# Optimization experiments

Measured on AMD Instinct MI355X. Metric: run time of the kernel, lower is better.

The kernel has to match this reference:

```python
import jax, jax.numpy as jnp
import numpy as np


def setup_inputs() -> dict:
    key = jax.random.key(0)
    ks = jax.random.split(key, 8)
    N, T, U = 8, 512, 64
    E, D, J, V = 512, 512, 512, 500
    s = 0.02
    return {
        "encoder_out": jax.random.normal(ks[0], (N, T, E), jnp.float32),
        "decoder_out": jax.random.normal(ks[1], (N, U, D), jnp.float32),
        "W_enc": jax.random.normal(ks[2], (J, E), jnp.float32) * s,
        "b_enc": jnp.zeros((J,), jnp.float32),
        "W_dec": jax.random.normal(ks[3], (J, D), jnp.float32) * s,
        "b_dec": jnp.zeros((J,), jnp.float32),
        "W_out": jax.random.normal(ks[4], (V, J), jnp.float32) * s,
        "b_out": jnp.zeros((V,), jnp.float32),
    }


def reference(encoder_out, decoder_out, W_enc, b_enc, W_dec, b_dec, W_out, b_out):
    # Project encoder [N,T,E]->[N,T,J] and decoder [N,U,D]->[N,U,J]
    enc = jnp.einsum("nte,je->ntj", encoder_out, W_enc) + b_enc
    dec = jnp.einsum("nud,jd->nuj", decoder_out, W_dec) + b_dec
    # Broadcast add over (T,U), tanh, then vocab projection -> [N,T,U,V]
    activations = jnp.tanh(enc[:, :, None, :] + dec[:, None, :, :])
    logits = jnp.einsum("ntuj,vj->ntuv", activations, W_out) + b_out
    return logits
```

## Files before the change

kernel.cpp:

```cpp
#include <hip/hip_runtime.h>
#include <hip/hip_bf16.h>


typedef __attribute__((ext_vector_type(4))) float f32x4;
typedef __attribute__((ext_vector_type(16))) float f32x16;
typedef __attribute__((ext_vector_type(4))) short s16x4;
typedef __attribute__((ext_vector_type(8))) short s16x8;
typedef __attribute__((ext_vector_type(8))) unsigned short u16x8;

static __device__ __forceinline__ unsigned short f2bf(float x) {
    union { float f; unsigned u; } v; v.f = x;
    return (unsigned short)((v.u + 0x7FFFu + ((v.u >> 16) & 1u)) >> 16);
}

static __device__ __forceinline__ float bf2f(unsigned short u) {
    union { unsigned u; float f; } v; v.u = ((unsigned)u) << 16;
    return v.f;
}

static __device__ __forceinline__ float fast_tanh(float x) {
    float e = __expf(2.0f * x);
    float r = __builtin_amdgcn_rcpf(e + 1.0f);
    return __builtin_fmaf(-2.0f, r, 1.0f);
}

static __device__ __forceinline__ void lbar() {
    asm volatile("s_waitcnt lgkmcnt(0)" ::: "memory");
    __builtin_amdgcn_s_barrier();
    __builtin_amdgcn_sched_barrier(0);
}

static __device__ __forceinline__ unsigned swz64(int r, int c) {
    return (unsigned)(r * 64 + ((c ^ ((r >> 1) & 3)) << 4));
}

static __device__ void proj_body(
    const float* __restrict__ A, const float* __restrict__ W,
    const float* __restrict__ b, unsigned short* __restrict__ C,
    int mt, int jt, unsigned short* As, unsigned short* Bs)
{
    const int tid = threadIdx.x;
    const int lane = tid & 63, wid = tid >> 6;
    const int wm = wid >> 1, wn = wid & 1;

    f32x4 acc[4][4];
    const f32x4 zero = {0.f, 0.f, 0.f, 0.f};
    #pragma unroll
    for (int i = 0; i < 4; ++i)
        #pragma unroll
        for (int j = 0; j < 4; ++j) acc[i][j] = zero;

    const int c8 = (tid & 7) * 8;
    const int rbase = tid >> 3;

    for (int kt = 0; kt < 8; ++kt) {
        __syncthreads();
        #pragma unroll
        for (int p = 0; p < 4; ++p) {
            int r = p * 32 + rbase;
            int byte = (r * 128 + c8 * 2) ^ ((r & 7) << 4);
            {
                const float* s = A + (size_t)(mt * 128 + r) * 512 + kt * 64 + c8;
                f32x4 v0 = *(const f32x4*)s, v1 = *(const f32x4*)(s + 4);
                s16x8 pk;
                pk[0] = (short)f2bf(v0[0]); pk[1] = (short)f2bf(v0[1]);
                pk[2] = (short)f2bf(v0[2]); pk[3] = (short)f2bf(v0[3]);
                pk[4] = (short)f2bf(v1[0]); pk[5] = (short)f2bf(v1[1]);
                pk[6] = (short)f2bf(v1[2]); pk[7] = (short)f2bf(v1[3]);
                *(s16x8*)((char*)As + byte) = pk;
            }
            {
                const float* s = W + (size_t)(jt * 128 + r) * 512 + kt * 64 + c8;
                f32x4 v0 = *(const f32x4*)s, v1 = *(const f32x4*)(s + 4);
                s16x8 pk;
                pk[0] = (short)f2bf(v0[0]); pk[1] = (short)f2bf(v0[1]);
                pk[2] = (short)f2bf(v0[2]); pk[3] = (short)f2bf(v0[3]);
                pk[4] = (short)f2bf(v1[0]); pk[5] = (short)f2bf(v1[1]);
                pk[6] = (short)f2bf(v1[2]); pk[7] = (short)f2bf(v1[3]);
                *(s16x8*)((char*)Bs + byte) = pk;
            }
        }
        __syncthreads();
        #pragma unroll
        for (int kk = 0; kk < 2; ++kk) {
            s16x8 af[4], bfr[4];
            #pragma unroll
            for (int mi = 0; mi < 4; ++mi) {
                int row = wm * 64 + mi * 16 + (lane & 15);
                int byte = (row * 128 + kk * 64 + ((lane >> 4) * 16)) ^ ((row & 7) << 4);
                af[mi] = *(const s16x8*)((const char*)As + byte);
            }
            #pragma unroll
            for (int ni = 0; ni < 4; ++ni) {
                int row = wn * 64 + ni * 16 + (lane & 15);
                int byte = (row * 128 + kk * 64 + ((lane >> 4) * 16)) ^ ((row & 7) << 4);
                bfr[ni] = *(const s16x8*)((const char*)Bs + byte);
            }
            #pragma unroll
            for (int mi = 0; mi < 4; ++mi)
                #pragma unroll
                for (int ni = 0; ni < 4; ++ni)
                    acc[mi][ni] = __builtin_amdgcn_mfma_f32_16x16x32_bf16(
                        af[mi], bfr[ni], acc[mi][ni], 0, 0, 0);
        }
    }

    #pragma unroll
    for (int ni = 0; ni < 4; ++ni) {
        int col = jt * 128 + wn * 64 + ni * 16 + (lane & 15);
        float bias = b[col];
        #pragma unroll
        for (int mi = 0; mi < 4; ++mi) {
            int row0 = mt * 128 + wm * 64 + mi * 16 + ((lane >> 4) << 2);
            #pragma unroll
            for (int j = 0; j < 4; ++j)
                C[(size_t)(row0 + j) * 512 + col] = f2bf(acc[mi][ni][j] + bias);
        }
    }
}

__global__ __launch_bounds__(256) void prep(
    const float* __restrict__ Wout, unsigned short* __restrict__ img,
    const float* __restrict__ encoder_out, const float* __restrict__ W_enc,
    const float* __restrict__ b_enc, unsigned short* __restrict__ enc_p,
    const float* __restrict__ decoder_out, const float* __restrict__ W_dec,
    const float* __restrict__ b_dec, unsigned short* __restrict__ dec_p,
    const float* __restrict__ b_out, float* __restrict__ bpad)
{
    __shared__ unsigned short As[128 * 64];
    __shared__ unsigned short Bs[128 * 64];
    const int b = blockIdx.x;
    if (b < 128) {
        int tid = b * 256 + threadIdx.x;
        int lane = tid & 63;
        int khalf = (tid >> 6) & 1;
        int tile = (tid >> 7) & 15;
        int kt = tid >> 11;
        int v = tile * 32 + (lane & 31);
        int k = kt * 32 + khalf * 16 + (lane >> 5) * 8;
        s16x8 pk = {0, 0, 0, 0, 0, 0, 0, 0};
        if (v < 500) {
            const float* s = Wout + (size_t)v * 512 + k;
            f32x4 a = *(const f32x4*)s, c = *(const f32x4*)(s + 4);
            pk[0] = (short)f2bf(a[0]); pk[1] = (short)f2bf(a[1]);
            pk[2] = (short)f2bf(a[2]); pk[3] = (short)f2bf(a[3]);
            pk[4] = (short)f2bf(c[0]); pk[5] = (short)f2bf(c[1]);
            pk[6] = (short)f2bf(c[2]); pk[7] = (short)f2bf(c[3]);
        }
        *(s16x8*)(img + (size_t)tid * 8) = pk;
    } else if (b < 256) {
        int q = b - 128;
        proj_body(encoder_out, W_enc, b_enc, enc_p, q & 31, q >> 5, As, Bs);
    } else if (b < 272) {
        int q = b - 256;
        proj_body(decoder_out, W_dec, b_dec, dec_p, q & 3, q >> 2, As, Bs);
    } else {
        int i = threadIdx.x;
        bpad[i] = (i < 500) ? b_out[i] : 0.f;
        bpad[i + 256] = (i + 256 < 500) ? b_out[i + 256] : 0.f;
    }
}

__global__ __launch_bounds__(256, 4) void joiner_main(
    const unsigned short* __restrict__ enc, const unsigned short* __restrict__ dec,
    const unsigned short* __restrict__ Wimg, const float* __restrict__ bout,
    float* __restrict__ out)
{
    __shared__ __align__(16) char raw[8192 + 16 * 260 * 4];
    unsigned short* As0 = (unsigned short*)raw;
    unsigned short* As1 = (unsigned short*)(raw + 4096);
    float* ep = (float*)(raw + 8192);

    const int bid = blockIdx.x;
    const int tid = threadIdx.x, lane = tid & 63, wn = tid >> 6;
    const int vt = bid & 1, t = (bid >> 1) & 511, n = bid >> 10;

    f32x16 acc[2][2];
    #pragma unroll
    for (int i = 0; i < 2; ++i)
        #pragma unroll
        for (int j = 0; j < 2; ++j)
            #pragma unroll
            for (int e = 0; e < 16; ++e) acc[i][j][e] = 0.f;

    const int r = tid >> 2;
    const int q = tid & 3;
    const unsigned short* erow = enc + ((size_t)n * 512 + t) * 512 + q * 8;
    const unsigned short* drow = dec + ((size_t)n * 64 + r) * 512 + q * 8;
    const unsigned abyte = swz64(r, q);
    const char* wbase = (const char*)Wimg + (size_t)(vt * 8 + wn * 2) * 2048
                        + (size_t)lane * 16;
    const int lr = lane & 31, kg = lane >> 5;

    s16x8 bc0, bc1, bc2, bc3;
    {
        u16x8 e = *(const u16x8*)erow;
        u16x8 d = *(const u16x8*)drow;
        s16x8 p;
        #pragma unroll
        for (int i = 0; i < 8; ++i)
            p[i] = (short)f2bf(fast_tanh(bf2f(e[i]) + bf2f(d[i])));
        *(s16x8*)((char*)As0 + abyte) = p;
        bc0 = *(const s16x8*)(wbase);
        bc1 = *(const s16x8*)(wbase + 1024);
        bc2 = *(const s16x8*)(wbase + 2048);
        bc3 = *(const s16x8*)(wbase + 3072);
    }
    lbar();

    #pragma unroll
    for (int kt = 0; kt < 16; ++kt) {
        const char* Ac = (char*)((kt & 1) ? As1 : As0);
        char* An = (char*)((kt & 1) ? As0 : As1);

        u16x8 eL, dL;
        if (kt < 15) {
            eL = *(const u16x8*)(erow + (kt + 1) * 32);
            dL = *(const u16x8*)(drow + (kt + 1) * 32);
        }
        s16x8 bn0, bn1, bn2, bn3;
        if (kt < 15) {
            const char* g = wbase + (size_t)(kt + 1) * 32768;
            bn0 = *(const s16x8*)(g);
            bn1 = *(const s16x8*)(g + 1024);
            bn2 = *(const s16x8*)(g + 2048);
            bn3 = *(const s16x8*)(g + 3072);
        }
        {
            s16x8 a0 = *(const s16x8*)(Ac + swz64(lr, kg));
            s16x8 a1 = *(const s16x8*)(Ac + swz64(32 + lr, kg));
            acc[0][0] = __builtin_amdgcn_mfma_f32_32x32x16_bf16(bc0, a0, acc[0][0], 0, 0, 0);
            acc[0][1] = __builtin_amdgcn_mfma_f32_32x32x16_bf16(bc2, a0, acc[0][1], 0, 0, 0);
            acc[1][0] = __builtin_amdgcn_mfma_f32_32x32x16_bf16(bc0, a1, acc[1][0], 0, 0, 0);
            acc[1][1] = __builtin_amdgcn_mfma_f32_32x32x16_bf16(bc2, a1, acc[1][1], 0, 0, 0);
            a0 = *(const s16x8*)(Ac + swz64(lr, 2 + kg));
            a1 = *(const s16x8*)(Ac + swz64(32 + lr, 2 + kg));
            acc[0][0] = __builtin_amdgcn_mfma_f32_32x32x16_bf16(bc1, a0, acc[0][0], 0, 0, 0);
            acc[0][1] = __builtin_amdgcn_mfma_f32_32x32x16_bf16(bc3, a0, acc[0][1], 0, 0, 0);
            acc[1][0] = __builtin_amdgcn_mfma_f32_32x32x16_bf16(bc1, a1, acc[1][0], 0, 0, 0);
            acc[1][1] = __builtin_amdgcn_mfma_f32_32x32x16_bf16(bc3, a1, acc[1][1], 0, 0, 0);
        }
        if (kt < 15) {
            s16x8 p;
            #pragma unroll
            for (int i = 0; i < 8; ++i)
                p[i] = (short)f2bf(fast_tanh(bf2f(eL[i]) + bf2f(dL[i])));
            *(s16x8*)(An + abyte) = p;
        }
        lbar();
        bc0 = bn0; bc1 = bn1; bc2 = bn2; bc3 = bn3;
    }

    const int hi4 = kg * 4;
    const size_t mg = ((size_t)n * 512 + t) * 64;
    #pragma unroll
    for (int o = 0; o < 4; ++o) {
        if (o) lbar();
        if ((lr >> 4) == (o & 1)) {
            const int mi = o >> 1;
            const int lrow = lr & 15;
            #pragma unroll
            for (int ni = 0; ni < 2; ++ni) {
                #pragma unroll
                for (int qq = 0; qq < 4; ++qq) {
                    int vloc = wn * 64 + ni * 32 + qq * 8 + hi4;
                    int v4 = vt * 256 + vloc;
                    if (v4 < 500) {
                        f32x4 b = *(const f32x4*)(bout + v4);
                        f32x4 ov;
                        ov[0] = acc[mi][ni][qq * 4 + 0] + b[0];
                        ov[1] = acc[mi][ni][qq * 4 + 1] + b[1];
                        ov[2] = acc[mi][ni][qq * 4 + 2] + b[2];
                        ov[3] = acc[mi][ni][qq * 4 + 3] + b[3];
                        *(f32x4*)(ep + lrow * 260 + vloc) = ov;
                    }
                }
            }
        }
        lbar();
        const int row0 = (o >> 1) * 32 + (o & 1) * 16;
        #pragma unroll
        for (int i = 0; i < 4; ++i) {
            int idx = i * 256 + tid;
            int rr = idx >> 6, ci = idx & 63;
            int v4 = vt * 256 + ci * 4;
            if (v4 < 500) {
                f32x4 ov = *(const f32x4*)(ep + rr * 260 + ci * 4);
                __builtin_nontemporal_store(
                    ov, (f32x4*)(out + (mg + row0 + rr) * 500 + v4));
            }
        }
    }
}

extern "C" void kernel_launch(void* const* d_in, const int* in_sizes, int n_in,
                              void* d_out, int out_size, void* d_ws, size_t ws_size,
                              hipStream_t stream) {
    const float* encoder_out = (const float*)d_in[0];
    const float* decoder_out = (const float*)d_in[1];
    const float* W_enc = (const float*)d_in[2];
    const float* b_enc = (const float*)d_in[3];
    const float* W_dec = (const float*)d_in[4];
    const float* b_dec = (const float*)d_in[5];
    const float* W_out = (const float*)d_in[6];
    const float* b_out = (const float*)d_in[7];
    float* out = (float*)d_out;

    unsigned short* enc_p = (unsigned short*)d_ws;
    unsigned short* dec_p = enc_p + (size_t)4096 * 512;
    unsigned short* wimg  = dec_p + (size_t)512 * 512;
    float* bpad = (float*)(wimg + 262144);

    prep<<<dim3(273), 256, 0, stream>>>(W_out, wimg,
                                        encoder_out, W_enc, b_enc, enc_p,
                                        decoder_out, W_dec, b_dec, dec_p,
                                        b_out, bpad);
    joiner_main<<<dim3(8192), 256, 0, stream>>>(enc_p, dec_p, wimg, bpad, out);
}
```

Baseline: 266.5 us.

## Enlarge joiner tile to 128x512 with 512 threads and deeper prefetch

The main kernel now covers two time steps by all 64 decoder positions and the full 512-wide vocab in each block, using 8 waves, instead of one time step and half the vocab. Each W_out fragment is reused across four M sub-tiles, and the tanh activation tile is built once for the whole vocab instead of once per vocab half. The encoder/decoder loads are now prefetched two k-steps ahead. The epilogue writes contiguous 32x500 output rows through a larger 66 KB LDS staging buffer that aliases the A buffers. This raises register and LDS use and cuts the grid to 2048 blocks, which may lower occupancy.

New measurement: 213.9 us, median of 2. 1.25x faster.

```diff
diff --git a/kernel.cpp b/kernel.cpp
--- a/kernel.cpp
+++ b/kernel.cpp
@@ -4,7 +4,6 @@
 
 typedef __attribute__((ext_vector_type(4))) float f32x4;
 typedef __attribute__((ext_vector_type(16))) float f32x16;
-typedef __attribute__((ext_vector_type(4))) short s16x4;
 typedef __attribute__((ext_vector_type(8))) short s16x8;
 typedef __attribute__((ext_vector_type(8))) unsigned short u16x8;
 
@@ -161,23 +160,23 @@
     }
 }
 
-__global__ __launch_bounds__(256, 4) void joiner_main(
+__global__ __launch_bounds__(512, 2) void joiner_main(
     const unsigned short* __restrict__ enc, const unsigned short* __restrict__ dec,
     const unsigned short* __restrict__ Wimg, const float* __restrict__ bout,
     float* __restrict__ out)
 {
-    __shared__ __align__(16) char raw[8192 + 16 * 260 * 4];
+    __shared__ __align__(16) char raw[66048];
     unsigned short* As0 = (unsigned short*)raw;
-    unsigned short* As1 = (unsigned short*)(raw + 4096);
-    float* ep = (float*)(raw + 8192);
+    unsigned short* As1 = (unsigned short*)(raw + 8192);
+    float* ep = (float*)raw;
 
     const int bid = blockIdx.x;
     const int tid = threadIdx.x, lane = tid & 63, wn = tid >> 6;
-    const int vt = bid & 1, t = (bid >> 1) & 511, n = bid >> 10;
-
-    f32x16 acc[2][2];
-    #pragma unroll
-    for (int i = 0; i < 2; ++i)
+    const int n = bid >> 8, tt = bid & 255;
+
+    f32x16 acc[4][2];
+    #pragma unroll
+    for (int i = 0; i < 4; ++i)
         #pragma unroll
         for (int j = 0; j < 2; ++j)
             #pragma unroll
@@ -185,14 +184,15 @@
 
     const int r = tid >> 2;
     const int q = tid & 3;
-    const unsigned short* erow = enc + ((size_t)n * 512 + t) * 512 + q * 8;
-    const unsigned short* drow = dec + ((size_t)n * 64 + r) * 512 + q * 8;
+    const int tl = r >> 6, u = r & 63;
+    const unsigned short* erow = enc + ((size_t)n * 512 + tt * 2 + tl) * 512 + q * 8;
+    const unsigned short* drow = dec + ((size_t)n * 64 + u) * 512 + q * 8;
     const unsigned abyte = swz64(r, q);
-    const char* wbase = (const char*)Wimg + (size_t)(vt * 8 + wn * 2) * 2048
-                        + (size_t)lane * 16;
+    const char* wbase = (const char*)Wimg + (size_t)wn * 4096 + (size_t)lane * 16;
     const int lr = lane & 31, kg = lane >> 5;
 
     s16x8 bc0, bc1, bc2, bc3;
+    u16x8 eN, dN;
     {
         u16x8 e = *(const u16x8*)erow;
         u16x8 d = *(const u16x8*)drow;
@@ -201,6 +201,8 @@
         for (int i = 0; i < 8; ++i)
             p[i] = (short)f2bf(fast_tanh(bf2f(e[i]) + bf2f(d[i])));
         *(s16x8*)((char*)As0 + abyte) = p;
+        eN = *(const u16x8*)(erow + 32);
+        dN = *(const u16x8*)(drow + 32);
         bc0 = *(const s16x8*)(wbase);
         bc1 = *(const s16x8*)(wbase + 1024);
         bc2 = *(const s16x8*)(wbase + 2048);
@@ -213,10 +215,16 @@
         const char* Ac = (char*)((kt & 1) ? As1 : As0);
         char* An = (char*)((kt & 1) ? As0 : As1);
 
-        u16x8 eL, dL;
         if (kt < 15) {
-            eL = *(const u16x8*)(erow + (kt + 1) * 32);
-            dL = *(const u16x8*)(drow + (kt + 1) * 32);
+            s16x8 p;
+            #pragma unroll
+            for (int i = 0; i < 8; ++i)
+                p[i] = (short)f2bf(fast_tanh(bf2f(eN[i]) + bf2f(dN[i])));
+            *(s16x8*)(An + abyte) = p;
+        }
+        if (kt < 14) {
+            eN = *(const u16x8*)(erow + (kt + 2) * 32);
+            dN = *(const u16x8*)(drow + (kt + 2) * 32);
         }
         s16x8 bn0, bn1, bn2, bn3;
         if (kt < 15) {
@@ -229,65 +237,68 @@
         {
             s16x8 a0 = *(const s16x8*)(Ac + swz64(lr, kg));
             s16x8 a1 = *(const s16x8*)(Ac + swz64(32 + lr, kg));
+            s16x8 a2 = *(const s16x8*)(Ac + swz64(64 + lr, kg));
+            s16x8 a3 = *(const s16x8*)(Ac + swz64(96 + lr, kg));
             acc[0][0] = __builtin_amdgcn_mfma_f32_32x32x16_bf16(bc0, a0, acc[0][0], 0, 0, 0);
             acc[0][1] = __builtin_amdgcn_mfma_f32_32x32x16_bf16(bc2, a0, acc[0][1], 0, 0, 0);
             acc[1][0] = __builtin_amdgcn_mfma_f32_32x32x16_bf16(bc0, a1, acc[1][0], 0, 0, 0);
             acc[1][1] = __builtin_amdgcn_mfma_f32_32x32x16_bf16(bc2, a1, acc[1][1], 0, 0, 0);
-            a0 = *(const s16x8*)(Ac + swz64(lr, 2 + kg));
-            a1 = *(const s16x8*)(Ac + swz64(32 + lr, 2 + kg));
+            acc[2][0] = __builtin_amdgcn_mfma_f32_32x32x16_bf16(bc0, a2, acc[2][0], 0, 0, 0);
+            acc[2][1] = __builtin_amdgcn_mfma_f32_32x32x16_bf16(bc2, a2, acc[2][1], 0, 0, 0);
+            acc[3][0] = __builtin_amdgcn_mfma_f32_32x32x16_bf16(bc0, a3, acc[3][0], 0, 0, 0);
+            acc[3][1] = __builtin_amdgcn_mfma_f32_32x32x16_bf16(bc2, a3, acc[3][1], 0, 0, 0);
+        }
+        {
+            s16x8 a0 = *(const s16x8*)(Ac + swz64(lr, 2 + kg));
+            s16x8 a1 = *(const s16x8*)(Ac + swz64(32 + lr, 2 + kg));
+            s16x8 a2 = *(const s16x8*)(Ac + swz64(64 + lr, 2 + kg));
+            s16x8 a3 = *(const s16x8*)(Ac + swz64(96 + lr, 2 + kg));
             acc[0][0] = __builtin_amdgcn_mfma_f32_32x32x16_bf16(bc1, a0, acc[0][0], 0, 0, 0);
             acc[0][1] = __builtin_amdgcn_mfma_f32_32x32x16_bf16(bc3, a0, acc[0][1], 0, 0, 0);
             acc[1][0] = __builtin_amdgcn_mfma_f32_32x32x16_bf16(bc1, a1, acc[1][0], 0, 0, 0);
             acc[1][1] = __builtin_amdgcn_mfma_f32_32x32x16_bf16(bc3, a1, acc[1][1], 0, 0, 0);
-        }
-        if (kt < 15) {
-            s16x8 p;
-            #pragma unroll
-            for (int i = 0; i < 8; ++i)
-                p[i] = (short)f2bf(fast_tanh(bf2f(eL[i]) + bf2f(dL[i])));
-            *(s16x8*)(An + abyte) = p;
+            acc[2][0] = __builtin_amdgcn_mfma_f32_32x32x16_bf16(bc1, a2, acc[2][0], 0, 0, 0);
+            acc[2][1] = __builtin_amdgcn_mfma_f32_32x32x16_bf16(bc3, a2, acc[2][1], 0, 0, 0);
+            acc[3][0] = __builtin_amdgcn_mfma_f32_32x32x16_bf16(bc1, a3, acc[3][0], 0, 0, 0);
+            acc[3][1] = __builtin_amdgcn_mfma_f32_32x32x16_bf16(bc3, a3, acc[3][1], 0, 0, 0);
         }
         lbar();
         bc0 = bn0; bc1 = bn1; bc2 = bn2; bc3 = bn3;
     }
 
     const int hi4 = kg * 4;
-    const size_t mg = ((size_t)n * 512 + t) * 64;
     #pragma unroll
     for (int o = 0; o < 4; ++o) {
         if (o) lbar();
-        if ((lr >> 4) == (o & 1)) {
-            const int mi = o >> 1;
-            const int lrow = lr & 15;
+        {
             #pragma unroll
             for (int ni = 0; ni < 2; ++ni) {
                 #pragma unroll
                 for (int qq = 0; qq < 4; ++qq) {
-                    int vloc = wn * 64 + ni * 32 + qq * 8 + hi4;
-                    int v4 = vt * 256 + vloc;
+                    int v4 = wn * 64 + ni * 32 + qq * 8 + hi4;
                     if (v4 < 500) {
                         f32x4 b = *(const f32x4*)(bout + v4);
                         f32x4 ov;
-                        ov[0] = acc[mi][ni][qq * 4 + 0] + b[0];
-                        ov[1] = acc[mi][ni][qq * 4 + 1] + b[1];
-                        ov[2] = acc[mi][ni][qq * 4 + 2] + b[2];
-                        ov[3] = acc[mi][ni][qq * 4 + 3] + b[3];
-                        *(f32x4*)(ep + lrow * 260 + vloc) = ov;
+                        ov[0] = acc[o][ni][qq * 4 + 0] + b[0];
+                        ov[1] = acc[o][ni][qq * 4 + 1] + b[1];
+                        ov[2] = acc[o][ni][qq * 4 + 2] + b[2];
+                        ov[3] = acc[o][ni][qq * 4 + 3] + b[3];
+                        *(f32x4*)(ep + lr * 516 + v4) = ov;
                     }
                 }
             }
         }
         lbar();
-        const int row0 = (o >> 1) * 32 + (o & 1) * 16;
-        #pragma unroll
-        for (int i = 0; i < 4; ++i) {
-            int idx = i * 256 + tid;
-            int rr = idx >> 6, ci = idx & 63;
-            int v4 = vt * 256 + ci * 4;
-            if (v4 < 500) {
-                f32x4 ov = *(const f32x4*)(ep + rr * 260 + ci * 4);
-                __builtin_nontemporal_store(
-                    ov, (f32x4*)(out + (mg + row0 + rr) * 500 + v4));
+        const size_t base =
+            (((size_t)n * 512 + tt * 2 + (o >> 1)) * 64 + (o & 1) * 32) * 500;
+        #pragma unroll
+        for (int i = 0; i < 8; ++i) {
+            int idx = i * 512 + tid;
+            if (idx < 4000) {
+                int rr = idx / 125;
+                int vi = (idx - rr * 125) * 4;
+                f32x4 ov = *(const f32x4*)(ep + rr * 516 + vi);
+                __builtin_nontemporal_store(ov, (f32x4*)(out + base + (size_t)idx * 4));
             }
         }
     }
@@ -315,5 +326,5 @@
                                         encoder_out, W_enc, b_enc, enc_p,
                                         decoder_out, W_dec, b_dec, dec_p,
                                         b_out, bpad);
-    joiner_main<<<dim3(8192), 256, 0, stream>>>(enc_p, dec_p, wimg, bpad, out);
-}
+    joiner_main<<<dim3(2048), 512, 0, stream>>>(enc_p, dec_p, wimg, bpad, out);
+}
```
